# Kernel optimization log

Hardware: AMD Instinct MI355X
Metric: run time of the kernel (lower is better)

## Reference

```python
import jax, jax.numpy as jnp
import numpy as np

BN_EPS = 1e-5

def setup_inputs() -> dict:
    key = jax.random.key(0)
    ks = jax.random.split(key, 8)
    B, N, d_in, d_out, M, K = 16, 16384, 64, 128, 4096, 16
    pos = jax.random.normal(ks[0], (B, N, 3), dtype=jnp.float32)
    feat = jax.random.normal(ks[1], (B, N, d_in), dtype=jnp.float32)
    fps_preprocess = jax.random.randint(ks[2], (B, M), 0, N, dtype=jnp.int64)
    k_idx = jax.random.randint(ks[3], (B, M, K), 0, N, dtype=jnp.int64)
    W = jax.random.normal(ks[4], (d_out, d_in), dtype=jnp.float32) / np.sqrt(d_in)
    b = jax.random.normal(ks[5], (d_out,), dtype=jnp.float32) * 0.01
    gamma = jnp.ones((d_out,), dtype=jnp.float32)
    beta = jnp.zeros((d_out,), dtype=jnp.float32)
    return {"pos": pos, "feat": feat, "fps_preprocess": fps_preprocess,
            "k_idx": k_idx, "W": W, "b": b, "gamma": gamma, "beta": beta}

def reference(pos, feat, fps_preprocess, k_idx, W, b, gamma, beta):
    B = pos.shape[0]
    # Linear: [B,N,d_in] @ [d_in,d_out] -> [B,N,d_out]
    h = jnp.einsum('bnd,od->bno', feat, W) + b
    # BatchNorm1d over channels (batch stats, biased variance) + ReLU
    mu = jnp.mean(h, axis=(0, 1))
    var = jnp.mean(jnp.square(h - mu), axis=(0, 1))
    h = jax.nn.relu(gamma * (h - mu) * jax.lax.rsqrt(var + BN_EPS) + beta)
    # Downsample positions via FPS indices: [B,M,3]
    pos_ds = jnp.take_along_axis(pos, fps_preprocess[:, :, None], axis=1)
    # Batched kNN gather [B,M,K,d_out] then max over neighbors
    bidx = jnp.arange(B)[:, None, None]
    feat_knn = h[bidx, k_idx]            # [B,M,K,d_out]
    feat_ds = jnp.max(feat_knn, axis=2)  # [B,M,d_out]
    return (pos_ds, feat_ds)
```

## Files before the change

### kernel.cpp

```cpp
#include <hip/hip_runtime.h>
#include <hip/hip_bf16.h>
#include <stdint.h>

typedef float f4 __attribute__((ext_vector_type(4)));
typedef float f32x4v __attribute__((ext_vector_type(4)));
typedef float f32x16 __attribute__((ext_vector_type(16)));
typedef short bf16x8 __attribute__((ext_vector_type(8)));
typedef unsigned int u32x2 __attribute__((ext_vector_type(2)));

static constexpr int Bc = 16, Nc = 16384, DIN = 64, DOUT = 128, Mc = 4096, KNN = 16;
static constexpr long Rr = (long)Bc * Nc;
static constexpr float EPS = 1e-5f;
static constexpr int POS_OUT = Bc * Mc * 3;
static constexpr int GBLK = 512;
static constexpr int PSTRIDE = 4160;
static constexpr int RGRP = 32;
static constexpr int CG_STRIDE = 8224;

__device__ __forceinline__ uint32_t cvt2(float a, float b) {
    union { __hip_bfloat162 h; uint32_t u; } c;
    c.h = __float22bfloat162_rn(make_float2(a, b));
    return c.u;
}

__global__ __launch_bounds__(256) void k_gram(const float* __restrict__ feat,
                                              unsigned short* __restrict__ feat16,
                                              float* __restrict__ part)
{
    __shared__ alignas(16) char lds[4 * CG_STRIDE];
    const int t = threadIdx.x;
    const int lane = t & 63;
    const int w = t >> 6;
    const long R0 = (long)blockIdx.x * 512;
    const f4* feat4 = (const f4*)feat;
    const unsigned lds_base = (unsigned)(size_t)&lds[0];

    f32x4v acc[4][4];
#pragma unroll
    for (int mi = 0; mi < 4; ++mi)
#pragma unroll
        for (int mj = 0; mj < 4; ++mj) acc[mi][mj] = (f32x4v){0.f, 0.f, 0.f, 0.f};
    f4 csum = (f4){0.f, 0.f, 0.f, 0.f};

    f4 v[16];
#pragma unroll
    for (int i = 0; i < 16; ++i)
        v[i] = feat4[R0 * 16 + t + i * 256];

    const int c4 = t & 15;
    const int cg = c4 >> 2;

    for (int ch = 0; ch < 2; ++ch) {
#pragma unroll
        for (int i = 0; i < 16; ++i) {
            int row = (t + i * 256) >> 4;
            uint2 pk = {cvt2(v[i][0], v[i][1]), cvt2(v[i][2], v[i][3])};
            csum += v[i];
            *(uint2*)(feat16 + (size_t)(R0 + ch * 256 + row) * 64 + c4 * 4) = pk;
            *(uint2*)(lds + cg * CG_STRIDE + row * 32 + (c4 & 3) * 8) = pk;
        }
        __syncthreads();
        if (ch == 0) {
#pragma unroll
            for (int i = 0; i < 16; ++i)
                v[i] = feat4[(R0 + 256) * 16 + t + i * 256];
        }
#pragma unroll
        for (int s = 0; s < 2; ++s) {
            const unsigned base = lds_base + (unsigned)((w * 2 + s) * 32 * 32 + lane * 8);
            u32x2 r0[4], r1[4];
#pragma unroll
            for (int g = 0; g < 4; ++g) {
                unsigned a = base + g * CG_STRIDE;
                asm volatile("ds_read_b64_tr_b16 %0, %2 offset:0\n\t"
                             "ds_read_b64_tr_b16 %1, %2 offset:512"
                             : "=v"(r0[g]), "=v"(r1[g]) : "v"(a));
            }
            asm volatile("s_waitcnt lgkmcnt(0)" ::: "memory");
            __builtin_amdgcn_sched_barrier(0);
            bf16x8 f[4];
#pragma unroll
            for (int g = 0; g < 4; ++g) {
                union { u32x2 p[2]; bf16x8 v8; } u;
                u.p[0] = r0[g]; u.p[1] = r1[g];
                f[g] = u.v8;
            }
#pragma unroll
            for (int mi = 0; mi < 4; ++mi)
#pragma unroll
                for (int mj = 0; mj < 4; ++mj)
                    acc[mi][mj] = __builtin_amdgcn_mfma_f32_16x16x32_bf16(
                        f[mi], f[mj], acc[mi][mj], 0, 0, 0);
        }
        __syncthreads();
    }

    float* fbuf = (float*)lds;
    ((f4*)fbuf)[t] = csum;
    __syncthreads();
    float* pb = part + (size_t)blockIdx.x * PSTRIDE;
    if (t < 16) {
        f4 s = (f4){0.f, 0.f, 0.f, 0.f};
#pragma unroll
        for (int q = 0; q < 16; ++q) s += ((f4*)fbuf)[q * 16 + t];
        ((f4*)pb)[t] = s;
    }
    __syncthreads();
    float* buf = fbuf + (w & 1) * 4096;
    const int lcol = lane & 15, lrow4 = (lane >> 4) * 4;
    if (w < 2) {
#pragma unroll
        for (int mi = 0; mi < 4; ++mi)
#pragma unroll
            for (int mj = 0; mj < 4; ++mj)
#pragma unroll
                for (int rg = 0; rg < 4; ++rg)
                    buf[(mi * 16 + lrow4 + rg) * 64 + mj * 16 + lcol] = acc[mi][mj][rg];
    }
    __syncthreads();
    if (w >= 2) {
#pragma unroll
        for (int mi = 0; mi < 4; ++mi)
#pragma unroll
            for (int mj = 0; mj < 4; ++mj)
#pragma unroll
                for (int rg = 0; rg < 4; ++rg)
                    buf[(mi * 16 + lrow4 + rg) * 64 + mj * 16 + lcol] += acc[mi][mj][rg];
    }
    __syncthreads();
#pragma unroll
    for (int q = 0; q < 16; ++q) {
        int e = t + q * 256;
        pb[64 + e] = fbuf[e] + fbuf[4096 + e];
    }
}

__global__ __launch_bounds__(256) void k_reduce1(const float* __restrict__ part,
                                                 float* __restrict__ part2)
{
    const int gid = blockIdx.x * 256 + threadIdx.x;
    const int grp = blockIdx.y;
    if (gid >= PSTRIDE) return;
    const float* pp = part + (size_t)grp * (GBLK / RGRP) * PSTRIDE + gid;
    float s[8];
#pragma unroll
    for (int j = 0; j < 8; ++j) s[j] = 0.f;
#pragma unroll
    for (int i = 0; i < GBLK / RGRP; i += 8)
#pragma unroll
        for (int j = 0; j < 8; ++j)
            s[j] += pp[(size_t)(i + j) * PSTRIDE];
    part2[(size_t)grp * PSTRIDE + gid] =
        ((s[0] + s[1]) + (s[2] + s[3])) + ((s[4] + s[5]) + (s[6] + s[7]));
}

__global__ __launch_bounds__(256) void k_reduce2(const float* __restrict__ part2,
                                                 float* __restrict__ stats)
{
    const int gid = blockIdx.x * 256 + threadIdx.x;
    if (gid >= PSTRIDE) return;
    float s[8];
#pragma unroll
    for (int j = 0; j < 8; ++j) s[j] = 0.f;
#pragma unroll
    for (int i = 0; i < RGRP; i += 8)
#pragma unroll
        for (int j = 0; j < 8; ++j)
            s[j] += part2[(size_t)(i + j) * PSTRIDE + gid];
    stats[gid] = ((s[0] + s[1]) + (s[2] + s[3])) + ((s[4] + s[5]) + (s[6] + s[7]));
}

__global__ __launch_bounds__(256) void k_gram_at(const float* __restrict__ feat,
                                                 float* __restrict__ stats)
{
    __shared__ float tile[64 * 64];
    f4* tile4 = (f4*)tile;
    const f4* feat4 = (const f4*)feat;
    const int t = threadIdx.x;
    const int i0 = (t >> 4) << 2;
    const int j0 = (t & 15) << 2;
    float acc[16];
#pragma unroll
    for (int k = 0; k < 16; ++k) acc[k] = 0.f;
    float csum = 0.f;
    for (int c = 0; c < 8; ++c) {
        const int base4 = (blockIdx.x * 512 + c * 64) * 16;
        __syncthreads();
#pragma unroll
        for (int k = 0; k < 4; ++k) tile4[t + k * 256] = feat4[base4 + t + k * 256];
        __syncthreads();
        for (int r = 0; r < 64; ++r) {
            f4 fi = tile4[r * 16 + (i0 >> 2)];
            f4 fj = tile4[r * 16 + (j0 >> 2)];
#pragma unroll
            for (int ii = 0; ii < 4; ++ii)
#pragma unroll
                for (int jj = 0; jj < 4; ++jj)
                    acc[ii * 4 + jj] = fmaf(fi[ii], fj[jj], acc[ii * 4 + jj]);
        }
        if (t < 64) {
            for (int r = 0; r < 64; ++r) csum += tile[r * 64 + t];
        }
    }
#pragma unroll
    for (int ii = 0; ii < 4; ++ii)
#pragma unroll
        for (int jj = 0; jj < 4; ++jj)
            atomicAdd(&stats[64 + (i0 + ii) * 64 + (j0 + jj)], acc[ii * 4 + jj]);
    if (t < 64) atomicAdd(&stats[t], csum);
}

__global__ __launch_bounds__(64) void k_stats(const float* __restrict__ stats,
                                              const float* __restrict__ W,
                                              const float* __restrict__ gamma,
                                              const float* __restrict__ beta,
                                              float* __restrict__ ST)
{
    const int o = blockIdx.x;
    const int i = threadIdx.x;
    __shared__ float wrow[64];
    wrow[i] = W[o * 64 + i];
    __syncthreads();
    const float* G = stats + 64;
    float inner = 0.f;
    for (int j = 0; j < 64; ++j) inner = fmaf(G[i * 64 + j], wrow[j], inner);
    float qi = inner * wrow[i];
    float cwi = stats[i] * wrow[i];
#pragma unroll
    for (int off = 32; off > 0; off >>= 1) {
        qi += __shfl_down(qi, off);
        cwi += __shfl_down(cwi, off);
    }
    if (i == 0) {
        const double invR = 1.0 / (double)Rr;
        double meanr = (double)cwi * invR;
        double var = (double)qi * invR - meanr * meanr;
        float s = gamma[o] / sqrtf((float)var + EPS);
        ST[o] = s;
        ST[DOUT + o] = beta[o] - (float)meanr * s;
    }
}

__global__ __launch_bounds__(512) void k_gmax(const unsigned short* __restrict__ feat16,
                                              const float* __restrict__ W,
                                              const float* __restrict__ ST,
                                              const int* __restrict__ kidx,
                                              const int* __restrict__ fps,
                                              const float* __restrict__ pos,
                                              float* __restrict__ out)
{
    __shared__ char lW[16 * 1024];
    __shared__ char lA[8][4096];
    const int t = threadIdx.x;
    const f4* W4 = (const f4*)W;
#pragma unroll
    for (int i = 0; i < 4; ++i) {
        int idx = t + i * 512;
        int row = idx >> 4, c4 = idx & 15;
        f4 v = W4[idx];
        uint2 pk = {cvt2(v[0], v[1]), cvt2(v[2], v[3])};
        *(uint2*)(lW + row * 128 + ((c4 * 8) ^ ((row & 7) << 4))) = pk;
    }

    const int lane = t & 63;
    const int w = t >> 6;
    const int l31 = lane & 31;
    const int hi = lane >> 5;
    const int lg = lane >> 3;
    const int lc = lane & 7;

    const int x = blockIdx.x & 7;
    const int k0 = blockIdx.x >> 3;

    char* myA = lA[w];

    float sc[4], tc[4];
#pragma unroll
    for (int cg = 0; cg < 4; ++cg) {
        sc[cg] = ST[cg * 32 + l31];
        tc[cg] = ST[DOUT + cg * 32 + l31];
    }

    int batch = x + 8 * (k0 >> 8);
    int p0n = batch * Mc + (k0 & 255) * 16 + w * 2;
    int idsn = __builtin_nontemporal_load(&kidx[p0n * KNN + l31]);

    __syncthreads();

    for (int cc = k0; cc < 512; cc += 96) {
        const int batchc = x + 8 * (cc >> 8);
        const char* fbp = (const char*)feat16 + (size_t)batchc * Nc * 128;
        const int p0 = p0n;
        const int ids = idsn;
        if (cc + 96 < 512) {
            int b2 = x + 8 * ((cc + 96) >> 8);
            p0n = b2 * Mc + ((cc + 96) & 255) * 16 + w * 2;
            idsn = __builtin_nontemporal_load(&kidx[p0n * KNN + l31]);
        }

        f4 g[4];
#pragma unroll
        for (int i2 = 0; i2 < 4; ++i2) {
            int rid = __shfl(ids, i2 * 8 + lg);
            g[i2] = *(const f4*)(fbp + (size_t)rid * 128 + lc * 16);
        }
#pragma unroll
        for (int i2 = 0; i2 < 4; ++i2) {
            int rsrc = i2 * 8 + lg;
            *(f4*)(myA + rsrc * 128 + ((lc * 16) ^ ((rsrc & 7) << 4))) = g[i2];
        }

        if (l31 < 3) {
            int p = p0 + hi;
            int id2 = fps[p];
            __builtin_nontemporal_store(pos[((size_t)batchc * Nc + id2) * 3 + l31],
                                        &out[p * 3 + l31]);
        }

        bf16x8 A[4];
#pragma unroll
        for (int ks = 0; ks < 4; ++ks)
            A[ks] = *(const bf16x8*)(myA + l31 * 128 +
                                     ((hi * 16 + ks * 32) ^ ((l31 & 7) << 4)));

#pragma unroll
        for (int cg = 0; cg < 4; ++cg) {
            const int row = cg * 32 + l31;
            f32x16 acc = {};
            __builtin_amdgcn_s_setprio(1);
#pragma unroll
            for (int ks = 0; ks < 4; ++ks) {
                bf16x8 wfv = *(const bf16x8*)(lW + row * 128 +
                                              ((ks * 32 + hi * 16) ^ ((row & 7) << 4)));
                acc = __builtin_amdgcn_mfma_f32_32x32x16_bf16(A[ks], wfv, acc, 0, 0, 0);
            }
            __builtin_amdgcn_s_setprio(0);
            float vmA = fmaxf(fmaxf(fmaxf(acc[0], acc[1]), fmaxf(acc[2], acc[3])),
                              fmaxf(fmaxf(acc[4], acc[5]), fmaxf(acc[6], acc[7])));
            float vmB = fmaxf(fmaxf(fmaxf(acc[8], acc[9]), fmaxf(acc[10], acc[11])),
                              fmaxf(fmaxf(acc[12], acc[13]), fmaxf(acc[14], acc[15])));
            vmA = fmaxf(vmA, __shfl_xor(vmA, 32));
            vmB = fmaxf(vmB, __shfl_xor(vmB, 32));
            float vsel = hi ? vmB : vmA;
            __builtin_nontemporal_store(
                fmaxf(fmaf(vsel, sc[cg], tc[cg]), 0.f),
                &out[POS_OUT + (size_t)(p0 + hi) * DOUT + cg * 32 + l31]);
        }
    }
}

__global__ __launch_bounds__(128) void k_gather_rc(const float* __restrict__ feat,
                                                   const float* __restrict__ W,
                                                   const float* __restrict__ ST,
                                                   const int* __restrict__ kidx,
                                                   const int* __restrict__ fps,
                                                   const float* __restrict__ pos,
                                                   float* __restrict__ out)
{
    __shared__ float frow[KNN][DIN];
    const int p = blockIdx.x;
    const int o = threadIdx.x;
    const int b = p >> 12;
    const f4* featf = (const f4*)feat;
    f4* frow4 = (f4*)frow;
#pragma unroll
    for (int q = 0; q < 2; ++q) {
        int jj = o + q * 128;
        int row = jj >> 4, i4 = jj & 15;
        int id = kidx[p * KNN + row];
        frow4[jj] = featf[((size_t)b * Nc + id) * 16 + i4];
    }
    __syncthreads();
    float wreg[64];
#pragma unroll
    for (int i4 = 0; i4 < 16; ++i4) {
        f4 wv = ((const f4*)W)[o * 16 + i4];
        wreg[i4 * 4 + 0] = wv[0];
        wreg[i4 * 4 + 1] = wv[1];
        wreg[i4 * 4 + 2] = wv[2];
        wreg[i4 * 4 + 3] = wv[3];
    }
    const float s = ST[o], tt = ST[DOUT + o];
    float vm = 0.f;
    for (int k = 0; k < KNN; ++k) {
        float acc = 0.f;
#pragma unroll
        for (int i = 0; i < 64; ++i) acc = fmaf(frow[k][i], wreg[i], acc);
        vm = fmaxf(vm, fmaf(acc, s, tt));
    }
    out[POS_OUT + (size_t)p * DOUT + o] = vm;
    if (o < 3) {
        int id = fps[p];
        out[p * 3 + o] = pos[((size_t)b * Nc + id) * 3 + o];
    }
}

extern "C" void kernel_launch(void* const* d_in, const int* in_sizes, int n_in,
                              void* d_out, int out_size, void* d_ws, size_t ws_size,
                              hipStream_t stream)
{
    const float* pos   = (const float*)d_in[0];
    const float* feat  = (const float*)d_in[1];
    const int*   fps   = (const int*)d_in[2];
    const int*   kidx  = (const int*)d_in[3];
    const float* W     = (const float*)d_in[4];
    const float* gamma = (const float*)d_in[6];
    const float* beta  = (const float*)d_in[7];
    float* out = (float*)d_out;

    float* stats = (float*)d_ws;
    float* ST = stats + PSTRIDE;
    const size_t F16_OFF = 32768;
    const size_t F16_BYTES = (size_t)Rr * DIN * 2;
    unsigned short* feat16 = (unsigned short*)((char*)d_ws + F16_OFF);
    float* part  = (float*)((char*)d_ws + F16_OFF + F16_BYTES);
    float* part2 = part + (size_t)GBLK * PSTRIDE;
    const size_t need = F16_OFF + F16_BYTES +
                        (size_t)(GBLK + RGRP) * PSTRIDE * 4;

    if (ws_size >= need) {
        k_gram<<<GBLK, 256, 0, stream>>>(feat, feat16, part);
        k_reduce1<<<dim3((PSTRIDE + 255) / 256, RGRP), 256, 0, stream>>>(part, part2);
        k_reduce2<<<(PSTRIDE + 255) / 256, 256, 0, stream>>>(part2, stats);
        k_stats<<<DOUT, 64, 0, stream>>>(stats, W, gamma, beta, ST);
        k_gmax<<<768, 512, 0, stream>>>(feat16, W, ST, kidx, fps, pos, out);
    } else {
        hipMemsetAsync(d_ws, 0, PSTRIDE * 4, stream);
        k_gram_at<<<512, 256, 0, stream>>>(feat, stats);
        k_stats<<<DOUT, 64, 0, stream>>>(stats, W, gamma, beta, ST);
        k_gather_rc<<<Bc * Mc, 128, 0, stream>>>(feat, W, ST, kidx, fps, pos, out);
    }
}
```

Baseline: 66.62 us.

## Load gathered rows directly into MFMA registers with double-buffered prefetch

The gather kernel no longer stages gathered feature rows through LDS with a swizzled write and read-back. Each lane now loads its bf16 fragment straight from global memory into MFMA operand registers. A two-stage register double buffer prefetches the next point group's rows while the current group's MFMAs run. The grid drops from 768 to 512 blocks, each doing a fixed 8 iterations with stride 8192 points. This cuts LDS traffic and frees shared memory, at the cost of more registers and less coalesced global loads, since each lane reads 16-byte pieces of scattered rows.

```diff
diff --git a/kernel.cpp b/kernel.cpp
--- a/kernel.cpp
+++ b/kernel.cpp
@@ -250,7 +250,6 @@
                                               float* __restrict__ out)
 {
     __shared__ char lW[16 * 1024];
-    __shared__ char lA[8][4096];
     const int t = threadIdx.x;
     const f4* W4 = (const f4*)W;
 #pragma unroll
@@ -266,13 +265,7 @@
     const int w = t >> 6;
     const int l31 = lane & 31;
     const int hi = lane >> 5;
-    const int lg = lane >> 3;
-    const int lc = lane & 7;
-
-    const int x = blockIdx.x & 7;
-    const int k0 = blockIdx.x >> 3;
-
-    char* myA = lA[w];
+    const int bl = blockIdx.x;
 
     float sc[4], tc[4];
 #pragma unroll
@@ -281,47 +274,48 @@
         tc[cg] = ST[DOUT + cg * 32 + l31];
     }
 
-    int batch = x + 8 * (k0 >> 8);
-    int p0n = batch * Mc + (k0 & 255) * 16 + w * 2;
-    int idsn = __builtin_nontemporal_load(&kidx[p0n * KNN + l31]);
-
-    __syncthreads();
-
-    for (int cc = k0; cc < 512; cc += 96) {
-        const int batchc = x + 8 * (cc >> 8);
-        const char* fbp = (const char*)feat16 + (size_t)batchc * Nc * 128;
-        const int p0 = p0n;
-        const int ids = idsn;
-        if (cc + 96 < 512) {
-            int b2 = x + 8 * ((cc + 96) >> 8);
-            p0n = b2 * Mc + ((cc + 96) & 255) * 16 + w * 2;
-            idsn = __builtin_nontemporal_load(&kidx[p0n * KNN + l31]);
-        }
-
-        f4 g[4];
-#pragma unroll
-        for (int i2 = 0; i2 < 4; ++i2) {
-            int rid = __shfl(ids, i2 * 8 + lg);
-            g[i2] = *(const f4*)(fbp + (size_t)rid * 128 + lc * 16);
-        }
-#pragma unroll
-        for (int i2 = 0; i2 < 4; ++i2) {
-            int rsrc = i2 * 8 + lg;
-            *(f4*)(myA + rsrc * 128 + ((lc * 16) ^ ((rsrc & 7) << 4))) = g[i2];
+    int p_next = bl * 16 + w * 2;
+    int ids_next = __builtin_nontemporal_load(&kidx[p_next * KNN + l31]);
+
+    __syncthreads();
+
+    bf16x8 A[2][4];
+    {
+        int bn = p_next >> 12;
+        const unsigned short* rp = feat16 + (size_t)bn * Nc * 64 +
+                                   (size_t)ids_next * 64 + hi * 8;
+#pragma unroll
+        for (int ks = 0; ks < 4; ++ks) A[0][ks] = *(const bf16x8*)(rp + ks * 16);
+    }
+    int p_cur = p_next;
+    p_next += 8192;
+    ids_next = __builtin_nontemporal_load(&kidx[p_next * KNN + l31]);
+
+#pragma unroll
+    for (int ph = 0; ph < 8; ++ph) {
+        const int cur = ph & 1;
+        const int pc = p_cur;
+        const int batchc = pc >> 12;
+
+        if (ph < 7) {
+            int bn = p_next >> 12;
+            const unsigned short* rp = feat16 + (size_t)bn * Nc * 64 +
+                                       (size_t)ids_next * 64 + hi * 8;
+#pragma unroll
+            for (int ks = 0; ks < 4; ++ks) A[cur ^ 1][ks] = *(const bf16x8*)(rp + ks * 16);
+            p_cur = p_next;
+            if (ph < 6) {
+                p_next += 8192;
+                ids_next = __builtin_nontemporal_load(&kidx[p_next * KNN + l31]);
+            }
         }
 
         if (l31 < 3) {
-            int p = p0 + hi;
+            int p = pc + hi;
             int id2 = fps[p];
             __builtin_nontemporal_store(pos[((size_t)batchc * Nc + id2) * 3 + l31],
                                         &out[p * 3 + l31]);
         }
-
-        bf16x8 A[4];
-#pragma unroll
-        for (int ks = 0; ks < 4; ++ks)
-            A[ks] = *(const bf16x8*)(myA + l31 * 128 +
-                                     ((hi * 16 + ks * 32) ^ ((l31 & 7) << 4)));
 
 #pragma unroll
         for (int cg = 0; cg < 4; ++cg) {
@@ -332,7 +326,7 @@
             for (int ks = 0; ks < 4; ++ks) {
                 bf16x8 wfv = *(const bf16x8*)(lW + row * 128 +
                                               ((ks * 32 + hi * 16) ^ ((row & 7) << 4)));
-                acc = __builtin_amdgcn_mfma_f32_32x32x16_bf16(A[ks], wfv, acc, 0, 0, 0);
+                acc = __builtin_amdgcn_mfma_f32_32x32x16_bf16(A[cur][ks], wfv, acc, 0, 0, 0);
             }
             __builtin_amdgcn_s_setprio(0);
             float vmA = fmaxf(fmaxf(fmaxf(acc[0], acc[1]), fmaxf(acc[2], acc[3])),
@@ -344,7 +338,7 @@
             float vsel = hi ? vmB : vmA;
             __builtin_nontemporal_store(
                 fmaxf(fmaf(vsel, sc[cg], tc[cg]), 0.f),
-                &out[POS_OUT + (size_t)(p0 + hi) * DOUT + cg * 32 + l31]);
+                &out[POS_OUT + (size_t)(pc + hi) * DOUT + cg * 32 + l31]);
         }
     }
 }
@@ -423,7 +417,7 @@
         k_reduce1<<<dim3((PSTRIDE + 255) / 256, RGRP), 256, 0, stream>>>(part, part2);
         k_reduce2<<<(PSTRIDE + 255) / 256, 256, 0, stream>>>(part2, stats);
         k_stats<<<DOUT, 64, 0, stream>>>(stats, W, gamma, beta, ST);
-        k_gmax<<<768, 512, 0, stream>>>(feat16, W, ST, kidx, fps, pos, out);
+        k_gmax<<<512, 512, 0, stream>>>(feat16, W, ST, kidx, fps, pos, out);
     } else {
         hipMemsetAsync(d_ws, 0, PSTRIDE * 4, stream);
         k_gram_at<<<512, 256, 0, stream>>>(feat, stats);
```

New measurement: 63.78 us (median of 2 runs). 1.04x faster.
